# Performance work log

Hardware: AMD Instinct MI355X
Metric: run time of the kernel (lower is better)

Reference implementation:

```python
import jax, jax.numpy as jnp
import numpy as np

B, N = 4, 2048
INPUT_DIM, KDIM, VDIM = 128, 128, 16
EMBED, V_EMBED, H = 128, 128, 8
HEAD_DIM = EMBED // H          # 16
V_HEAD_DIM = V_EMBED // H      # 16 (== VDIM, required by the torch view)
SCALING = HEAD_DIM ** -0.5


def setup_inputs() -> dict:
    key = jax.random.key(0)
    ks = jax.random.split(key, 12)
    inp = {
        "query": jax.random.normal(ks[0], (B, N, INPUT_DIM), dtype=jnp.float32),
        "key": jax.random.normal(ks[1], (B, N, KDIM), dtype=jnp.float32),
        "value": jax.random.normal(ks[2], (B, N, VDIM), dtype=jnp.float32),
        # nn.Linear weights are [out, in]; init.normal_ -> std normal
        "Wq": jax.random.normal(ks[3], (EMBED, INPUT_DIM), dtype=jnp.float32),
        "bq": jnp.zeros((EMBED,), dtype=jnp.float32),
        "Wk": jax.random.normal(ks[4], (EMBED, KDIM), dtype=jnp.float32),
        "bk": jnp.zeros((EMBED,), dtype=jnp.float32),
        "Wv": jax.random.normal(ks[5], (V_EMBED, VDIM), dtype=jnp.float32),
        "bv": jnp.zeros((V_EMBED,), dtype=jnp.float32),
        "Wo": jax.random.normal(ks[6], (V_EMBED // H, V_EMBED), dtype=jnp.float32),
        "bo": jnp.zeros((V_EMBED // H,), dtype=jnp.float32),
    }
    return inp


def reference(query, key, value, Wq, bq, Wk, bk, Wv, bv, Wo, bo):
    # projections
    q = (query @ Wq.T + bq) * SCALING                 # [B, N, EMBED]
    k = key @ Wk.T + bk                               # [B, N, EMBED]
    v = value @ Wv.T + bv                             # [B, N, V_EMBED]
    # split heads: [B, H, N, head_dim]
    q = q.reshape(B, N, H, HEAD_DIM).transpose(0, 2, 1, 3)
    k = k.reshape(B, N, H, HEAD_DIM).transpose(0, 2, 1, 3)
    v = v.reshape(B, N, H, V_HEAD_DIM).transpose(0, 2, 1, 3)
    # full NxN scores (naive attention, as in the source)
    scores = jnp.einsum("bhnd,bhmd->bhnm", q, k)      # [B, H, N, N]
    attn = jax.nn.softmax(scores, axis=-1)
    # dropout is identity in eval mode
    ctx = jnp.einsum("bhnm,bhme->bhne", attn, v)      # [B, H, N, V_HEAD_DIM]
    ctx = ctx.transpose(0, 2, 1, 3).reshape(B, N, V_EMBED)
    out = ctx @ Wo.T + bo                             # [B, N, V_EMBED // H]
    return out
```

## Files before the change

kernel.cpp:

```cpp
#include <hip/hip_runtime.h>
#include <hip/hip_bf16.h>
#include <math.h>

typedef unsigned short ushort_t;
typedef unsigned int uint_t;
typedef __bf16 bf16x8 __attribute__((ext_vector_type(8)));
typedef float f32x4 __attribute__((ext_vector_type(4)));
typedef __fp16 fp16v2 __attribute__((ext_vector_type(2)));
typedef _Float16 f16x4 __attribute__((ext_vector_type(4)));

#define NSEQ 2048
#define QSCALE 0.3606737602222409f

__device__ __forceinline__ float exp2_fast(float x) {
#if __has_builtin(__builtin_amdgcn_exp2f)
    return __builtin_amdgcn_exp2f(x);
#else
    return exp2f(x);
#endif
}

union U8 { ushort_t u[8]; bf16x8 v; uint4 q; uint_t w[4]; };
union F8 { float f[8]; float4 v4[2]; };
union H4 { fp16v2 h2[2]; f16x4 v; uint_t w[2]; };
union HV { fp16v2 h2[4]; uint4 q; };

__device__ __forceinline__ uint_t pk2(float a, float b) {
    __hip_bfloat162 h2 = __float22bfloat162_rn(make_float2(a, b));
    union { __hip_bfloat162 h; uint_t u; } cv; cv.h = h2; return cv.u;
}

__device__ __forceinline__ void split8(const F8& x, U8& hi, U8& lo) {
#pragma unroll
    for (int p = 0; p < 4; ++p) {
        const float a = x.f[2*p], b = x.f[2*p+1];
        const uint_t hw = pk2(a, b);
        hi.w[p] = hw;
        const float ha = __uint_as_float(hw << 16);
        const float hb = __uint_as_float(hw & 0xFFFF0000u);
        lo.w[p] = pk2(a - ha, b - hb);
    }
}

__global__ __launch_bounds__(256) void wpack_kernel(
    const float* __restrict__ Wq, const float* __restrict__ Wk,
    const float* __restrict__ Wo,
    ushort_t* __restrict__ wpk_hi, ushort_t* __restrict__ wpk_lo,
    ushort_t* __restrict__ wo_hi, ushort_t* __restrict__ wo_lo)
{
    const int idx = blockIdx.x * 256 + threadIdx.x;
    if (idx < 4096) {
        const int lane = idx & 63;
        const int f    = (idx >> 6) & 3;
        const int ct   = (idx >> 8) & 7;
        const int mat  = idx >> 11;
        const float* W = mat ? Wk : Wq;
        const float* src = W + (size_t)(ct * 16 + (lane & 15)) * 128
                             + f * 32 + (lane >> 4) * 8;
        F8 x; x.v4[0] = *(const float4*)src; x.v4[1] = *(const float4*)(src + 4);
        U8 hi, lo;
        split8(x, hi, lo);
        const size_t dst = (size_t)mat * 16384 + ((size_t)(ct * 4 + f) * 64 + lane) * 8;
        *(uint4*)(wpk_hi + dst) = hi.q;
        *(uint4*)(wpk_lo + dst) = lo.q;
    } else if (idx < 4352) {
        const int i2   = idx - 4096;
        const int lane = i2 & 63;
        const int f    = i2 >> 6;
        const float* src = Wo + (size_t)(lane & 15) * 128
                              + f * 32 + (lane >> 4) * 8;
        F8 x; x.v4[0] = *(const float4*)src; x.v4[1] = *(const float4*)(src + 4);
        U8 hi, lo;
        split8(x, hi, lo);
        const size_t dst = ((size_t)f * 64 + lane) * 8;
        *(uint4*)(wo_hi + dst) = hi.q;
        *(uint4*)(wo_lo + dst) = lo.q;
    }
}

__global__ __launch_bounds__(256, 2) void proj_kernel(
    const float* __restrict__ query, const float* __restrict__ key,
    const float* __restrict__ value,
    const float* __restrict__ bq, const float* __restrict__ bk,
    const float* __restrict__ Wv, const float* __restrict__ bv,
    const ushort_t* __restrict__ wpk_hi, const ushort_t* __restrict__ wpk_lo,
    ushort_t* __restrict__ q_hi, ushort_t* __restrict__ q_lo,
    ushort_t* __restrict__ k_hi, ushort_t* __restrict__ k_lo,
    ushort_t* __restrict__ vt)
{
    const int t   = threadIdx.x;
    const int w   = t >> 6;
    const int l   = t & 63;
    const int col = l & 15;
    const int g   = l >> 4;
    const int rbase = blockIdx.x * 16;
    const int b = rbase >> 11;

    const int isK    = w >> 1;
    const int cthalf = (w & 1) * 4;

    const float* X = isK ? key : query;
    const float* xrow = X + (size_t)(rbase + col) * 128 + g * 8;
    bf16x8 xh[4], xl[4];
#pragma unroll
    for (int f = 0; f < 4; ++f) {
        F8 x;
        x.v4[0] = *(const float4*)(xrow + f * 32);
        x.v4[1] = *(const float4*)(xrow + f * 32 + 4);
        U8 hi, lo;
        split8(x, hi, lo);
        xh[f] = hi.v; xl[f] = lo.v;
    }

    const float* bias = isK ? bk : bq;
    ushort_t* dhi = isK ? k_hi : q_hi;
    ushort_t* dlo = isK ? k_lo : q_lo;
    const float scale = isK ? 1.0f : QSCALE;
    const int tok = (rbase & 2047) + col;

#pragma unroll
    for (int ctl = 0; ctl < 4; ++ctl) {
        const int h = cthalf + ctl;
        bf16x8 whf[4], wlf[4];
#pragma unroll
        for (int f = 0; f < 4; ++f) {
            const size_t o = (size_t)isK * 16384
                           + ((size_t)(h * 4 + f) * 64 + l) * 8;
            whf[f] = *(const bf16x8*)(wpk_hi + o);
            wlf[f] = *(const bf16x8*)(wpk_lo + o);
        }
        const float4 b4 = *(const float4*)(bias + h * 16 + 4 * g);
        f32x4 acc = {b4.x, b4.y, b4.z, b4.w};
#pragma unroll
        for (int f = 0; f < 4; ++f) {
            acc = __builtin_amdgcn_mfma_f32_16x16x32_bf16(whf[f], xh[f], acc, 0, 0, 0);
            acc = __builtin_amdgcn_mfma_f32_16x16x32_bf16(wlf[f], xh[f], acc, 0, 0, 0);
            acc = __builtin_amdgcn_mfma_f32_16x16x32_bf16(whf[f], xl[f], acc, 0, 0, 0);
        }
        const size_t abase = ((size_t)(b * 8 + h) * NSEQ + tok) * 16 + 4 * g;
        const float a0 = acc[0]*scale, a1 = acc[1]*scale;
        const float a2 = acc[2]*scale, a3 = acc[3]*scale;
        const uint_t h01 = pk2(a0, a1), h23 = pk2(a2, a3);
        const uint_t l01 = pk2(a0 - __uint_as_float(h01 << 16),
                               a1 - __uint_as_float(h01 & 0xFFFF0000u));
        const uint_t l23 = pk2(a2 - __uint_as_float(h23 << 16),
                               a3 - __uint_as_float(h23 & 0xFFFF0000u));
        uint2 sh; sh.x = h01; sh.y = h23;
        uint2 sl; sl.x = l01; sl.y = l23;
        *(uint2*)(dhi + abase) = sh;
        *(uint2*)(dlo + abase) = sl;
    }

    const int e  = t & 127;
    const int rh = t >> 7;
    const int r0 = rbase + rh * 8;
    const float4* Wv4 = (const float4*)(Wv + (size_t)e * 16);
    const float4 wv0 = Wv4[0], wv1 = Wv4[1], wv2 = Wv4[2], wv3 = Wv4[3];
    const float bvv = bv[e];
    F8 af;
#pragma unroll
    for (int r = 0; r < 8; ++r) {
        const float4* xv4 = (const float4*)(value + (size_t)(r0 + r) * 16);
        const float4 x0 = xv4[0], x1 = xv4[1], x2 = xv4[2], x3 = xv4[3];
        float a = bvv;
        a += wv0.x*x0.x + wv0.y*x0.y + wv0.z*x0.z + wv0.w*x0.w;
        a += wv1.x*x1.x + wv1.y*x1.y + wv1.z*x1.z + wv1.w*x1.w;
        a += wv2.x*x2.x + wv2.y*x2.y + wv2.z*x2.z + wv2.w*x2.w;
        a += wv3.x*x3.x + wv3.y*x3.y + wv3.z*x3.z + wv3.w*x3.w;
        af.f[r] = a;
    }
    HV vpk;
#pragma unroll
    for (int p = 0; p < 4; ++p)
        vpk.h2[p] = __builtin_amdgcn_cvt_pkrtz(af.f[2*p], af.f[2*p+1]);
    const int hv = e >> 4, dd = e & 15;
    *(uint4*)(vt + ((size_t)(b * 8 + hv) * 16 + dd) * NSEQ + (r0 & 2047)) = vpk.q;
}

__global__ __launch_bounds__(256, 4) void attn_kernel(
    const ushort_t* __restrict__ q_hi, const ushort_t* __restrict__ q_lo,
    const ushort_t* __restrict__ k_hi, const ushort_t* __restrict__ k_lo,
    const ushort_t* __restrict__ vt, ushort_t* __restrict__ ctxb)
{
    const int t    = threadIdx.x;
    const int w    = t >> 6;
    const int l    = t & 63;
    const int col  = l & 15;
    const int g    = l >> 4;
    const int qsub = w & 1;
    const int kh   = w >> 1;

    const int id   = blockIdx.x;
    const int rest = id >> 3;
    const int bh   = (rest >> 5) * 8 + (id & 7);
    const int qbase = (rest & 31) * 64 + qsub * 32;

    __shared__ float lds_m[4][32];
    __shared__ __align__(16) float lds_o[2][2][16][16];
    __shared__ float lds_l[2][2][16];

    U8 Uz;
#pragma unroll
    for (int i = 0; i < 8; ++i) Uz.u[i] = 0;
    const bf16x8 zf = Uz.v;

    bf16x8 bq1[2], bq2[2];
#pragma unroll
    for (int s = 0; s < 2; ++s) {
        const size_t qoff = ((size_t)(bh * NSEQ + qbase + s * 16 + col)) * 16 + (g & 1) * 8;
        bq1[s] = *(const bf16x8*)(q_hi + qoff);
        const bf16x8 t2 = *(const bf16x8*)(q_lo + qoff);
        bq2[s] = (g < 2) ? t2 : zf;
    }

    const ushort_t* ksel = (g < 2) ? k_hi : k_lo;
    const ushort_t* aptr = ksel + ((size_t)bh * NSEQ + col) * 16 + (g & 1) * 8
                         + (size_t)kh * (1024 * 16);
    const ushort_t* vp = vt + ((size_t)bh * 16 + col) * NSEQ + kh * 1024;

    float m0 = -INFINITY, m1 = -INFINITY;
    const f32x4 z = {0.f, 0.f, 0.f, 0.f};
    bf16x8 pa1[2], pa2[2];
    pa1[0] = *(const bf16x8*)(aptr);
    pa2[0] = *(const bf16x8*)(aptr + 256);
    pa1[1] = *(const bf16x8*)(aptr + 512);
    pa2[1] = *(const bf16x8*)(aptr + 768);
#pragma unroll 2
    for (int kb = 0; kb < 32; ++kb) {
        const bf16x8 c1 = pa1[kb & 1], c2 = pa2[kb & 1];
        const int kn = (kb + 2) & 31;
        pa1[kb & 1] = *(const bf16x8*)(aptr + (size_t)kn * 512);
        pa2[kb & 1] = *(const bf16x8*)(aptr + (size_t)kn * 512 + 256);
        const f32x4 s1 = __builtin_amdgcn_mfma_f32_16x16x32_bf16(c1, bq1[0], z, 0, 0, 0);
        const f32x4 s2 = __builtin_amdgcn_mfma_f32_16x16x32_bf16(c2, bq1[0], z, 0, 0, 0);
        const f32x4 s3 = __builtin_amdgcn_mfma_f32_16x16x32_bf16(c1, bq1[1], z, 0, 0, 0);
        const f32x4 s4 = __builtin_amdgcn_mfma_f32_16x16x32_bf16(c2, bq1[1], z, 0, 0, 0);
        m0 = fmaxf(m0, fmaxf(fmaxf(s1[0], s1[1]), fmaxf(s1[2], s1[3])));
        m0 = fmaxf(m0, fmaxf(fmaxf(s2[0], s2[1]), fmaxf(s2[2], s2[3])));
        m1 = fmaxf(m1, fmaxf(fmaxf(s3[0], s3[1]), fmaxf(s3[2], s3[3])));
        m1 = fmaxf(m1, fmaxf(fmaxf(s4[0], s4[1]), fmaxf(s4[2], s4[3])));
    }
    m0 = fmaxf(m0, __shfl_xor(m0, 16)); m0 = fmaxf(m0, __shfl_xor(m0, 32));
    m1 = fmaxf(m1, __shfl_xor(m1, 16)); m1 = fmaxf(m1, __shfl_xor(m1, 32));
    if (l < 32) lds_m[w][l] = (l < 16) ? m0 : m1;
    __syncthreads();
    const float mf0 = fmaxf(m0, lds_m[w ^ 2][col]);
    const float mf1 = fmaxf(m1, lds_m[w ^ 2][col + 16]);
    const f32x4 zin0 = {-mf0, -mf0, -mf0, -mf0};
    const f32x4 zin1 = {-mf1, -mf1, -mf1, -mf1};

    f32x4 o0 = {0.f,0.f,0.f,0.f}, o1 = {0.f,0.f,0.f,0.f};
    float ls0 = 0.f, ls1 = 0.f;
    f16x4 pv1[2], pv2[2];
    pv1[0] = *(const f16x4*)(vp + g * 4);
    pv2[0] = *(const f16x4*)(vp + 16 + g * 4);
    pv1[1] = *(const f16x4*)(vp + 32 + g * 4);
    pv2[1] = *(const f16x4*)(vp + 48 + g * 4);

#pragma unroll 2
    for (int kb = 0; kb < 32; ++kb) {
        const bf16x8 c1 = pa1[kb & 1], c2 = pa2[kb & 1];
        const f16x4 v1 = pv1[kb & 1], v2 = pv2[kb & 1];
        const int kn = (kb + 2) & 31;
        pa1[kb & 1] = *(const bf16x8*)(aptr + (size_t)kn * 512);
        pa2[kb & 1] = *(const bf16x8*)(aptr + (size_t)kn * 512 + 256);
        pv1[kb & 1] = *(const f16x4*)(vp + kn * 32 + g * 4);
        pv2[kb & 1] = *(const f16x4*)(vp + kn * 32 + 16 + g * 4);

        {
            f32x4 st1 = __builtin_amdgcn_mfma_f32_16x16x32_bf16(c1, bq2[0], zin0, 0, 0, 0);
            st1       = __builtin_amdgcn_mfma_f32_16x16x32_bf16(c1, bq1[0], st1, 0, 0, 0);
            f32x4 st2 = __builtin_amdgcn_mfma_f32_16x16x32_bf16(c2, bq2[0], zin0, 0, 0, 0);
            st2       = __builtin_amdgcn_mfma_f32_16x16x32_bf16(c2, bq1[0], st2, 0, 0, 0);
            const float p0 = exp2_fast(st1[0]), p1 = exp2_fast(st1[1]);
            const float p2 = exp2_fast(st1[2]), p3 = exp2_fast(st1[3]);
            const float p4 = exp2_fast(st2[0]), p5 = exp2_fast(st2[1]);
            const float p6 = exp2_fast(st2[2]), p7 = exp2_fast(st2[3]);
            ls0 += ((p0 + p1) + (p2 + p3)) + ((p4 + p5) + (p6 + p7));
            H4 b1u, b2u;
            b1u.h2[0] = __builtin_amdgcn_cvt_pkrtz(p0, p1);
            b1u.h2[1] = __builtin_amdgcn_cvt_pkrtz(p2, p3);
            b2u.h2[0] = __builtin_amdgcn_cvt_pkrtz(p4, p5);
            b2u.h2[1] = __builtin_amdgcn_cvt_pkrtz(p6, p7);
            o0 = __builtin_amdgcn_mfma_f32_16x16x16f16(v1, b1u.v, o0, 0, 0, 0);
            o0 = __builtin_amdgcn_mfma_f32_16x16x16f16(v2, b2u.v, o0, 0, 0, 0);
        }
        {
            f32x4 st1 = __builtin_amdgcn_mfma_f32_16x16x32_bf16(c1, bq2[1], zin1, 0, 0, 0);
            st1       = __builtin_amdgcn_mfma_f32_16x16x32_bf16(c1, bq1[1], st1, 0, 0, 0);
            f32x4 st2 = __builtin_amdgcn_mfma_f32_16x16x32_bf16(c2, bq2[1], zin1, 0, 0, 0);
            st2       = __builtin_amdgcn_mfma_f32_16x16x32_bf16(c2, bq1[1], st2, 0, 0, 0);
            const float p0 = exp2_fast(st1[0]), p1 = exp2_fast(st1[1]);
            const float p2 = exp2_fast(st1[2]), p3 = exp2_fast(st1[3]);
            const float p4 = exp2_fast(st2[0]), p5 = exp2_fast(st2[1]);
            const float p6 = exp2_fast(st2[2]), p7 = exp2_fast(st2[3]);
            ls1 += ((p0 + p1) + (p2 + p3)) + ((p4 + p5) + (p6 + p7));
            H4 b1u, b2u;
            b1u.h2[0] = __builtin_amdgcn_cvt_pkrtz(p0, p1);
            b1u.h2[1] = __builtin_amdgcn_cvt_pkrtz(p2, p3);
            b2u.h2[0] = __builtin_amdgcn_cvt_pkrtz(p4, p5);
            b2u.h2[1] = __builtin_amdgcn_cvt_pkrtz(p6, p7);
            o1 = __builtin_amdgcn_mfma_f32_16x16x16f16(v1, b1u.v, o1, 0, 0, 0);
            o1 = __builtin_amdgcn_mfma_f32_16x16x16f16(v2, b2u.v, o1, 0, 0, 0);
        }
    }

    ls0 += __shfl_xor(ls0, 16); ls0 += __shfl_xor(ls0, 32);
    ls1 += __shfl_xor(ls1, 16); ls1 += __shfl_xor(ls1, 32);

    if (w >= 2) {
        *(f32x4*)&lds_o[w - 2][0][col][4 * g] = o0;
        *(f32x4*)&lds_o[w - 2][1][col][4 * g] = o1;
        if (l < 32) lds_l[w - 2][l >> 4][col] = (l < 16) ? ls0 : ls1;
    }
    __syncthreads();
    if (w < 2) {
        const int b = bh >> 3, h = bh & 7;
#pragma unroll
        for (int s = 0; s < 2; ++s) {
            const f32x4 ob = *(const f32x4*)&lds_o[w][s][col][4 * g];
            const f32x4 oa = s ? o1 : o0;
            const float lt = (s ? ls1 : ls0) + lds_l[w][s][col];
            const float li = 1.0f / lt;
            const float r0 = (oa[0] + ob[0]) * li;
            const float r1 = (oa[1] + ob[1]) * li;
            const float r2 = (oa[2] + ob[2]) * li;
            const float r3 = (oa[3] + ob[3]) * li;
            uint2 pkd; pkd.x = pk2(r0, r1); pkd.y = pk2(r2, r3);
            *(uint2*)(ctxb + ((size_t)(b * NSEQ + qbase + s * 16 + col)) * 128
                      + h * 16 + 4 * g) = pkd;
        }
    }
}

__global__ __launch_bounds__(64) void outproj_kernel(
    const ushort_t* __restrict__ ctxb,
    const ushort_t* __restrict__ wo_hi, const ushort_t* __restrict__ wo_lo,
    const float* __restrict__ bo, float* __restrict__ out)
{
    const int l   = threadIdx.x;
    const int col = l & 15;
    const int g   = l >> 4;
    const int row0 = blockIdx.x * 16;

    const float bval = bo[col];
    f32x4 acc = {bval, bval, bval, bval};
    const ushort_t* ar = ctxb + (size_t)(row0 + col) * 128 + g * 8;
#pragma unroll
    for (int f = 0; f < 4; ++f) {
        const bf16x8 a = *(const bf16x8*)(ar + f * 32);
        const size_t o = ((size_t)f * 64 + l) * 8;
        const bf16x8 bh_ = *(const bf16x8*)(wo_hi + o);
        const bf16x8 bl_ = *(const bf16x8*)(wo_lo + o);
        acc = __builtin_amdgcn_mfma_f32_16x16x32_bf16(a, bh_, acc, 0, 0, 0);
        acc = __builtin_amdgcn_mfma_f32_16x16x32_bf16(a, bl_, acc, 0, 0, 0);
    }
#pragma unroll
    for (int r = 0; r < 4; ++r)
        out[(size_t)(row0 + 4 * g + r) * 16 + col] = acc[r];
}

extern "C" void kernel_launch(void* const* d_in, const int* in_sizes, int n_in,
                              void* d_out, int out_size, void* d_ws, size_t ws_size,
                              hipStream_t stream)
{
    const float* query = (const float*)d_in[0];
    const float* key_  = (const float*)d_in[1];
    const float* value = (const float*)d_in[2];
    const float* Wq = (const float*)d_in[3];
    const float* bq = (const float*)d_in[4];
    const float* Wk = (const float*)d_in[5];
    const float* bk = (const float*)d_in[6];
    const float* Wv = (const float*)d_in[7];
    const float* bv = (const float*)d_in[8];
    const float* Wo = (const float*)d_in[9];
    const float* bo = (const float*)d_in[10];
    float* out = (float*)d_out;

    ushort_t* base = (ushort_t*)d_ws;
    ushort_t* q_hi = base;
    ushort_t* q_lo = base + (1u << 20);
    ushort_t* k_hi = base + (2u << 20);
    ushort_t* k_lo = base + (3u << 20);
    ushort_t* vt   = base + (4u << 20);
    ushort_t* ctxb = base + (5u << 20);
    ushort_t* wpk_hi = base + (6u << 20);
    ushort_t* wpk_lo = wpk_hi + 32768;
    ushort_t* wo_hi  = wpk_hi + 65536;
    ushort_t* wo_lo  = wo_hi + 2048;

    wpack_kernel<<<dim3(17), dim3(256), 0, stream>>>(
        Wq, Wk, Wo, wpk_hi, wpk_lo, wo_hi, wo_lo);
    proj_kernel<<<dim3(512), dim3(256), 0, stream>>>(
        query, key_, value, bq, bk, Wv, bv, wpk_hi, wpk_lo,
        q_hi, q_lo, k_hi, k_lo, vt);
    attn_kernel<<<dim3(1024), dim3(256), 0, stream>>>(
        q_hi, q_lo, k_hi, k_lo, vt, ctxb);
    outproj_kernel<<<dim3(512), dim3(64), 0, stream>>>(
        ctxb, wo_hi, wo_lo, bo, out);
}
```

Baseline: 135.4 us.

## Split projection kernel, deepen attention prefetch, compute row sums via MFMA

```diff
diff --git a/kernel.cpp b/kernel.cpp
--- a/kernel.cpp
+++ b/kernel.cpp
@@ -78,28 +78,27 @@
     }
 }
 
-__global__ __launch_bounds__(256, 2) void proj_kernel(
+__global__ __launch_bounds__(256, 4) void qk_proj_kernel(
     const float* __restrict__ query, const float* __restrict__ key,
-    const float* __restrict__ value,
     const float* __restrict__ bq, const float* __restrict__ bk,
-    const float* __restrict__ Wv, const float* __restrict__ bv,
     const ushort_t* __restrict__ wpk_hi, const ushort_t* __restrict__ wpk_lo,
     ushort_t* __restrict__ q_hi, ushort_t* __restrict__ q_lo,
-    ushort_t* __restrict__ k_hi, ushort_t* __restrict__ k_lo,
-    ushort_t* __restrict__ vt)
+    ushort_t* __restrict__ k_hi, ushort_t* __restrict__ k_lo)
 {
     const int t   = threadIdx.x;
     const int w   = t >> 6;
     const int l   = t & 63;
     const int col = l & 15;
     const int g   = l >> 4;
-    const int rbase = blockIdx.x * 16;
+
+    const int gw  = blockIdx.x * 4 + w;
+    const int mat = gw & 1;
+    const int h   = (gw >> 1) & 7;
+    const int T   = gw >> 4;
+    const int rbase = T * 16;
     const int b = rbase >> 11;
 
-    const int isK    = w >> 1;
-    const int cthalf = (w & 1) * 4;
-
-    const float* X = isK ? key : query;
+    const float* X = mat ? key : query;
     const float* xrow = X + (size_t)(rbase + col) * 128 + g * 8;
     bf16x8 xh[4], xl[4];
 #pragma unroll
@@ -112,45 +111,50 @@
         xh[f] = hi.v; xl[f] = lo.v;
     }
 
-    const float* bias = isK ? bk : bq;
-    ushort_t* dhi = isK ? k_hi : q_hi;
-    ushort_t* dlo = isK ? k_lo : q_lo;
-    const float scale = isK ? 1.0f : QSCALE;
+    bf16x8 whf[4], wlf[4];
+#pragma unroll
+    for (int f = 0; f < 4; ++f) {
+        const size_t o = (size_t)mat * 16384 + ((size_t)(h * 4 + f) * 64 + l) * 8;
+        whf[f] = *(const bf16x8*)(wpk_hi + o);
+        wlf[f] = *(const bf16x8*)(wpk_lo + o);
+    }
+
+    const float* bias = mat ? bk : bq;
+    const float4 b4 = *(const float4*)(bias + h * 16 + 4 * g);
+    f32x4 acc = {b4.x, b4.y, b4.z, b4.w};
+#pragma unroll
+    for (int f = 0; f < 4; ++f) {
+        acc = __builtin_amdgcn_mfma_f32_16x16x32_bf16(whf[f], xh[f], acc, 0, 0, 0);
+        acc = __builtin_amdgcn_mfma_f32_16x16x32_bf16(wlf[f], xh[f], acc, 0, 0, 0);
+        acc = __builtin_amdgcn_mfma_f32_16x16x32_bf16(whf[f], xl[f], acc, 0, 0, 0);
+    }
+
+    ushort_t* dhi = mat ? k_hi : q_hi;
+    ushort_t* dlo = mat ? k_lo : q_lo;
+    const float scale = mat ? 1.0f : QSCALE;
     const int tok = (rbase & 2047) + col;
-
-#pragma unroll
-    for (int ctl = 0; ctl < 4; ++ctl) {
-        const int h = cthalf + ctl;
-        bf16x8 whf[4], wlf[4];
-#pragma unroll
-        for (int f = 0; f < 4; ++f) {
-            const size_t o = (size_t)isK * 16384
-                           + ((size_t)(h * 4 + f) * 64 + l) * 8;
-            whf[f] = *(const bf16x8*)(wpk_hi + o);
-            wlf[f] = *(const bf16x8*)(wpk_lo + o);
-        }
-        const float4 b4 = *(const float4*)(bias + h * 16 + 4 * g);
-        f32x4 acc = {b4.x, b4.y, b4.z, b4.w};
-#pragma unroll
-        for (int f = 0; f < 4; ++f) {
-            acc = __builtin_amdgcn_mfma_f32_16x16x32_bf16(whf[f], xh[f], acc, 0, 0, 0);
-            acc = __builtin_amdgcn_mfma_f32_16x16x32_bf16(wlf[f], xh[f], acc, 0, 0, 0);
-            acc = __builtin_amdgcn_mfma_f32_16x16x32_bf16(whf[f], xl[f], acc, 0, 0, 0);
-        }
-        const size_t abase = ((size_t)(b * 8 + h) * NSEQ + tok) * 16 + 4 * g;
-        const float a0 = acc[0]*scale, a1 = acc[1]*scale;
-        const float a2 = acc[2]*scale, a3 = acc[3]*scale;
-        const uint_t h01 = pk2(a0, a1), h23 = pk2(a2, a3);
-        const uint_t l01 = pk2(a0 - __uint_as_float(h01 << 16),
-                               a1 - __uint_as_float(h01 & 0xFFFF0000u));
-        const uint_t l23 = pk2(a2 - __uint_as_float(h23 << 16),
-                               a3 - __uint_as_float(h23 & 0xFFFF0000u));
-        uint2 sh; sh.x = h01; sh.y = h23;
-        uint2 sl; sl.x = l01; sl.y = l23;
-        *(uint2*)(dhi + abase) = sh;
-        *(uint2*)(dlo + abase) = sl;
-    }
-
+    const size_t abase = ((size_t)(b * 8 + h) * NSEQ + tok) * 16 + 4 * g;
+    const float a0 = acc[0]*scale, a1 = acc[1]*scale;
+    const float a2 = acc[2]*scale, a3 = acc[3]*scale;
+    const uint_t h01 = pk2(a0, a1), h23 = pk2(a2, a3);
+    const uint_t l01 = pk2(a0 - __uint_as_float(h01 << 16),
+                           a1 - __uint_as_float(h01 & 0xFFFF0000u));
+    const uint_t l23 = pk2(a2 - __uint_as_float(h23 << 16),
+                           a3 - __uint_as_float(h23 & 0xFFFF0000u));
+    uint2 sh; sh.x = h01; sh.y = h23;
+    uint2 sl; sl.x = l01; sl.y = l23;
+    *(uint2*)(dhi + abase) = sh;
+    *(uint2*)(dlo + abase) = sl;
+}
+
+__global__ __launch_bounds__(256) void v_proj_kernel(
+    const float* __restrict__ value,
+    const float* __restrict__ Wv, const float* __restrict__ bv,
+    ushort_t* __restrict__ vt)
+{
+    const int t  = threadIdx.x;
+    const int rbase = blockIdx.x * 16;
+    const int b = rbase >> 11;
     const int e  = t & 127;
     const int rh = t >> 7;
     const int r0 = rbase + rh * 8;
@@ -220,17 +224,18 @@
 
     float m0 = -INFINITY, m1 = -INFINITY;
     const f32x4 z = {0.f, 0.f, 0.f, 0.f};
-    bf16x8 pa1[2], pa2[2];
-    pa1[0] = *(const bf16x8*)(aptr);
-    pa2[0] = *(const bf16x8*)(aptr + 256);
-    pa1[1] = *(const bf16x8*)(aptr + 512);
-    pa2[1] = *(const bf16x8*)(aptr + 768);
-#pragma unroll 2
+    bf16x8 pa1[4], pa2[4];
+#pragma unroll
+    for (int s = 0; s < 4; ++s) {
+        pa1[s] = *(const bf16x8*)(aptr + (size_t)s * 512);
+        pa2[s] = *(const bf16x8*)(aptr + (size_t)s * 512 + 256);
+    }
+#pragma unroll 4
     for (int kb = 0; kb < 32; ++kb) {
-        const bf16x8 c1 = pa1[kb & 1], c2 = pa2[kb & 1];
-        const int kn = (kb + 2) & 31;
-        pa1[kb & 1] = *(const bf16x8*)(aptr + (size_t)kn * 512);
-        pa2[kb & 1] = *(const bf16x8*)(aptr + (size_t)kn * 512 + 256);
+        const bf16x8 c1 = pa1[kb & 3], c2 = pa2[kb & 3];
+        const int kn = (kb + 4) & 31;
+        pa1[kb & 3] = *(const bf16x8*)(aptr + (size_t)kn * 512);
+        pa2[kb & 3] = *(const bf16x8*)(aptr + (size_t)kn * 512 + 256);
         const f32x4 s1 = __builtin_amdgcn_mfma_f32_16x16x32_bf16(c1, bq1[0], z, 0, 0, 0);
         const f32x4 s2 = __builtin_amdgcn_mfma_f32_16x16x32_bf16(c2, bq1[0], z, 0, 0, 0);
         const f32x4 s3 = __builtin_amdgcn_mfma_f32_16x16x32_bf16(c1, bq1[1], z, 0, 0, 0);
@@ -250,63 +255,58 @@
     const f32x4 zin1 = {-mf1, -mf1, -mf1, -mf1};
 
     f32x4 o0 = {0.f,0.f,0.f,0.f}, o1 = {0.f,0.f,0.f,0.f};
-    float ls0 = 0.f, ls1 = 0.f;
-    f16x4 pv1[2], pv2[2];
-    pv1[0] = *(const f16x4*)(vp + g * 4);
-    pv2[0] = *(const f16x4*)(vp + 16 + g * 4);
-    pv1[1] = *(const f16x4*)(vp + 32 + g * 4);
-    pv2[1] = *(const f16x4*)(vp + 48 + g * 4);
-
-#pragma unroll 2
+    f32x4 la0 = {0.f,0.f,0.f,0.f}, la1 = {0.f,0.f,0.f,0.f};
+    const f16x4 onesh = {(_Float16)1.f, (_Float16)1.f, (_Float16)1.f, (_Float16)1.f};
+    f16x4 pv1[4], pv2[4];
+#pragma unroll
+    for (int s = 0; s < 4; ++s) {
+        pv1[s] = *(const f16x4*)(vp + s * 32 + g * 4);
+        pv2[s] = *(const f16x4*)(vp + s * 32 + 16 + g * 4);
+    }
+
+#pragma unroll 4
     for (int kb = 0; kb < 32; ++kb) {
-        const bf16x8 c1 = pa1[kb & 1], c2 = pa2[kb & 1];
-        const f16x4 v1 = pv1[kb & 1], v2 = pv2[kb & 1];
-        const int kn = (kb + 2) & 31;
-        pa1[kb & 1] = *(const bf16x8*)(aptr + (size_t)kn * 512);
-        pa2[kb & 1] = *(const bf16x8*)(aptr + (size_t)kn * 512 + 256);
-        pv1[kb & 1] = *(const f16x4*)(vp + kn * 32 + g * 4);
-        pv2[kb & 1] = *(const f16x4*)(vp + kn * 32 + 16 + g * 4);
+        const bf16x8 c1 = pa1[kb & 3], c2 = pa2[kb & 3];
+        const f16x4 v1 = pv1[kb & 3], v2 = pv2[kb & 3];
+        const int kn = (kb + 4) & 31;
+        pa1[kb & 3] = *(const bf16x8*)(aptr + (size_t)kn * 512);
+        pa2[kb & 3] = *(const bf16x8*)(aptr + (size_t)kn * 512 + 256);
+        pv1[kb & 3] = *(const f16x4*)(vp + kn * 32 + g * 4);
+        pv2[kb & 3] = *(const f16x4*)(vp + kn * 32 + 16 + g * 4);
 
         {
             f32x4 st1 = __builtin_amdgcn_mfma_f32_16x16x32_bf16(c1, bq2[0], zin0, 0, 0, 0);
             st1       = __builtin_amdgcn_mfma_f32_16x16x32_bf16(c1, bq1[0], st1, 0, 0, 0);
             f32x4 st2 = __builtin_amdgcn_mfma_f32_16x16x32_bf16(c2, bq2[0], zin0, 0, 0, 0);
             st2       = __builtin_amdgcn_mfma_f32_16x16x32_bf16(c2, bq1[0], st2, 0, 0, 0);
-            const float p0 = exp2_fast(st1[0]), p1 = exp2_fast(st1[1]);
-            const float p2 = exp2_fast(st1[2]), p3 = exp2_fast(st1[3]);
-            const float p4 = exp2_fast(st2[0]), p5 = exp2_fast(st2[1]);
-            const float p6 = exp2_fast(st2[2]), p7 = exp2_fast(st2[3]);
-            ls0 += ((p0 + p1) + (p2 + p3)) + ((p4 + p5) + (p6 + p7));
             H4 b1u, b2u;
-            b1u.h2[0] = __builtin_amdgcn_cvt_pkrtz(p0, p1);
-            b1u.h2[1] = __builtin_amdgcn_cvt_pkrtz(p2, p3);
-            b2u.h2[0] = __builtin_amdgcn_cvt_pkrtz(p4, p5);
-            b2u.h2[1] = __builtin_amdgcn_cvt_pkrtz(p6, p7);
-            o0 = __builtin_amdgcn_mfma_f32_16x16x16f16(v1, b1u.v, o0, 0, 0, 0);
-            o0 = __builtin_amdgcn_mfma_f32_16x16x16f16(v2, b2u.v, o0, 0, 0, 0);
+            b1u.h2[0] = __builtin_amdgcn_cvt_pkrtz(exp2_fast(st1[0]), exp2_fast(st1[1]));
+            b1u.h2[1] = __builtin_amdgcn_cvt_pkrtz(exp2_fast(st1[2]), exp2_fast(st1[3]));
+            b2u.h2[0] = __builtin_amdgcn_cvt_pkrtz(exp2_fast(st2[0]), exp2_fast(st2[1]));
+            b2u.h2[1] = __builtin_amdgcn_cvt_pkrtz(exp2_fast(st2[2]), exp2_fast(st2[3]));
+            o0  = __builtin_amdgcn_mfma_f32_16x16x16f16(v1,    b1u.v, o0,  0, 0, 0);
+            la0 = __builtin_amdgcn_mfma_f32_16x16x16f16(onesh, b1u.v, la0, 0, 0, 0);
+            o0  = __builtin_amdgcn_mfma_f32_16x16x16f16(v2,    b2u.v, o0,  0, 0, 0);
+            la0 = __builtin_amdgcn_mfma_f32_16x16x16f16(onesh, b2u.v, la0, 0, 0, 0);
         }
         {
             f32x4 st1 = __builtin_amdgcn_mfma_f32_16x16x32_bf16(c1, bq2[1], zin1, 0, 0, 0);
             st1       = __builtin_amdgcn_mfma_f32_16x16x32_bf16(c1, bq1[1], st1, 0, 0, 0);
             f32x4 st2 = __builtin_amdgcn_mfma_f32_16x16x32_bf16(c2, bq2[1], zin1, 0, 0, 0);
             st2       = __builtin_amdgcn_mfma_f32_16x16x32_bf16(c2, bq1[1], st2, 0, 0, 0);
-            const float p0 = exp2_fast(st1[0]), p1 = exp2_fast(st1[1]);
-            const float p2 = exp2_fast(st1[2]), p3 = exp2_fast(st1[3]);
-            const float p4 = exp2_fast(st2[0]), p5 = exp2_fast(st2[1]);
-            const float p6 = exp2_fast(st2[2]), p7 = exp2_fast(st2[3]);
-            ls1 += ((p0 + p1) + (p2 + p3)) + ((p4 + p5) + (p6 + p7));
             H4 b1u, b2u;
-            b1u.h2[0] = __builtin_amdgcn_cvt_pkrtz(p0, p1);
-            b1u.h2[1] = __builtin_amdgcn_cvt_pkrtz(p2, p3);
-            b2u.h2[0] = __builtin_amdgcn_cvt_pkrtz(p4, p5);
-            b2u.h2[1] = __builtin_amdgcn_cvt_pkrtz(p6, p7);
-            o1 = __builtin_amdgcn_mfma_f32_16x16x16f16(v1, b1u.v, o1, 0, 0, 0);
-            o1 = __builtin_amdgcn_mfma_f32_16x16x16f16(v2, b2u.v, o1, 0, 0, 0);
+            b1u.h2[0] = __builtin_amdgcn_cvt_pkrtz(exp2_fast(st1[0]), exp2_fast(st1[1]));
+            b1u.h2[1] = __builtin_amdgcn_cvt_pkrtz(exp2_fast(st1[2]), exp2_fast(st1[3]));
+            b2u.h2[0] = __builtin_amdgcn_cvt_pkrtz(exp2_fast(st2[0]), exp2_fast(st2[1]));
+            b2u.h2[1] = __builtin_amdgcn_cvt_pkrtz(exp2_fast(st2[2]), exp2_fast(st2[3]));
+            o1  = __builtin_amdgcn_mfma_f32_16x16x16f16(v1,    b1u.v, o1,  0, 0, 0);
+            la1 = __builtin_amdgcn_mfma_f32_16x16x16f16(onesh, b1u.v, la1, 0, 0, 0);
+            o1  = __builtin_amdgcn_mfma_f32_16x16x16f16(v2,    b2u.v, o1,  0, 0, 0);
+            la1 = __builtin_amdgcn_mfma_f32_16x16x16f16(onesh, b2u.v, la1, 0, 0, 0);
         }
     }
 
-    ls0 += __shfl_xor(ls0, 16); ls0 += __shfl_xor(ls0, 32);
-    ls1 += __shfl_xor(ls1, 16); ls1 += __shfl_xor(ls1, 32);
+    const float ls0 = la0[0], ls1 = la1[0];
 
     if (w >= 2) {
         *(f32x4*)&lds_o[w - 2][0][col][4 * g] = o0;
@@ -391,9 +391,9 @@
 
     wpack_kernel<<<dim3(17), dim3(256), 0, stream>>>(
         Wq, Wk, Wo, wpk_hi, wpk_lo, wo_hi, wo_lo);
-    proj_kernel<<<dim3(512), dim3(256), 0, stream>>>(
-        query, key_, value, bq, bk, Wv, bv, wpk_hi, wpk_lo,
-        q_hi, q_lo, k_hi, k_lo, vt);
+    v_proj_kernel<<<dim3(512), dim3(256), 0, stream>>>(value, Wv, bv, vt);
+    qk_proj_kernel<<<dim3(2048), dim3(256), 0, stream>>>(
+        query, key_, bq, bk, wpk_hi, wpk_lo, q_hi, q_lo, k_hi, k_lo);
     attn_kernel<<<dim3(1024), dim3(256), 0, stream>>>(
         q_hi, q_lo, k_hi, k_lo, vt, ctxb);
     outproj_kernel<<<dim3(512), dim3(64), 0, stream>>>(
```

Result: slower. 143.9 us (+6.3%).
